# Kernel optimization log

Measured on AMD Instinct MI355X. Metric: run time of the kernel, lower is better.

The kernel has to match this reference:

```python
import jax, jax.numpy as jnp
import numpy as np
from jax import lax

B, N = 8, 32768
N_G, N_C, K = 256, 64, 16
n_G, k_ = 16, 4          # sqrt(N_G), sqrt(K)
M, m_ = N_G * K, n_G * k_
EPS = 1e-6


def _w(key, i, o):
    return jax.random.normal(key, (i, o), jnp.float32) * (1.0 / np.sqrt(i))


def setup_inputs() -> dict:
    key = jax.random.key(0)
    ks = jax.random.split(key, 16)
    return {
        "pts": jax.random.normal(ks[0], (B, N, 3), jnp.float32),
        # G2SD: PointNet encoder (3->128->256, maxpool) + folding decoder (2+256 -> 256 -> 3)
        "ge_w1": _w(ks[1], 3, 128),   "ge_b1": jnp.zeros((128,), jnp.float32),
        "ge_w2": _w(ks[2], 128, 256), "ge_b2": jnp.zeros((256,), jnp.float32),
        "gd_w1": _w(ks[3], 258, 256), "gd_b1": jnp.zeros((256,), jnp.float32),
        "gd_w2": _w(ks[4], 256, 3),   "gd_b2": jnp.zeros((3,), jnp.float32),
        # S2PF: per-point encoder (3->128, maxpool) + per-point flattener (3+128 -> 128 -> 2)
        "se_w1": _w(ks[5], 3, 128),   "se_b1": jnp.zeros((128,), jnp.float32),
        "sd_w1": _w(ks[6], 131, 128), "sd_b1": jnp.zeros((128,), jnp.float32),
        "sd_w2": _w(ks[7], 128, 2),   "sd_b2": jnp.zeros((2,), jnp.float32),
    }


def _sqdist(a, b):
    # a [B,P,3], b [B,Q,3] -> [B,P,Q]
    return (jnp.sum(a * a, -1)[:, :, None] + jnp.sum(b * b, -1)[:, None, :]
            - 2.0 * jnp.einsum('bpd,bqd->bpq', a, b))


def fps(pts, n):
    Bb, Nn, _ = pts.shape
    def step(carry, _):
        dist, cur = carry
        sel = pts[jnp.arange(Bb), cur]                       # [B,3]
        d = jnp.sum((pts - sel[:, None, :]) ** 2, -1)        # [B,N]
        dist = jnp.minimum(dist, d)
        nxt = jnp.argmax(dist, -1).astype(jnp.int32)
        return (dist, nxt), cur
    init = (jnp.full((Bb, Nn), 1e10, pts.dtype), jnp.zeros((Bb,), jnp.int32))
    _, idx = lax.scan(step, init, None, length=n)            # [n,B]
    return idx.T                                             # [B,n]


def index_points(pts, idx):
    # pts [B,N,3], idx [B,...] -> [B,...,3]
    return jax.vmap(lambda p, i: p[i])(pts, idx)


def _grid(nn):
    lin = (jnp.arange(nn, dtype=jnp.float32) + 0.5) / nn
    gy, gx = jnp.meshgrid(lin, lin, indexing='ij')
    return jnp.stack([gx, gy], -1).reshape(nn * nn, 2)       # row-major [nn*nn,2]


def g2sd(pts_g, ge_w1, ge_b1, ge_w2, ge_b2, gd_w1, gd_b1, gd_w2, gd_b2):
    h = jax.nn.relu(pts_g @ ge_w1 + ge_b1)
    h = jax.nn.relu(h @ ge_w2 + ge_b2)
    code = jnp.max(h, axis=1)                                # [B,256]
    grid = jnp.broadcast_to(_grid(n_G)[None], (pts_g.shape[0], N_G, 2))
    feat = jnp.concatenate([grid, jnp.broadcast_to(code[:, None, :], (pts_g.shape[0], N_G, 256))], -1)
    h2 = jax.nn.relu(feat @ gd_w1 + gd_b1)
    return h2 @ gd_w2 + gd_b2                                # [B,N_G,3]


def s2pf(x, se_w1, se_b1, sd_w1, sd_b1, sd_w2, sd_b2):
    # x [BG, N_C, 3] -> 2D embedding [BG, N_C, 2]
    h = jax.nn.relu(x @ se_w1 + se_b1)
    code = jnp.max(h, axis=1)                                # [BG,128]
    f = jnp.concatenate([x, jnp.broadcast_to(code[:, None, :], (x.shape[0], x.shape[1], 128))], -1)
    h2 = jax.nn.relu(f @ sd_w1 + sd_b1)
    return h2 @ sd_w2 + sd_b2


def normalize_anchor_patches(pts_c):
    c = jnp.mean(pts_c, axis=2, keepdims=True)
    x = pts_c - c
    s = jnp.max(jnp.linalg.norm(x, axis=-1), axis=-1)[..., None, None]
    return x / (s + 1e-8)


def rescale_pe(pe, lo, hi):
    mn = jnp.min(pe, axis=1, keepdims=True)
    mx = jnp.max(pe, axis=1, keepdims=True)
    return (pe - mn) / (mx - mn + 1e-8) * (hi - lo) + lo


def reference(pts, ge_w1, ge_b1, ge_w2, ge_b2, gd_w1, gd_b1, gd_w2, gd_b2,
              se_w1, se_b1, sd_w1, sd_b1, sd_w2, sd_b2):
    Bb = pts.shape[0]
    # 1) FPS -> anchor points, G2SD -> grid-ordered reconstruction
    pts_g = index_points(pts, fps(pts, N_G))                 # [B,N_G,3]
    rec_g = g2sd(pts_g, ge_w1, ge_b1, ge_w2, ge_b2, gd_w1, gd_b1, gd_w2, gd_b2)
    # 2) KNN patches around each grid anchor
    d = _sqdist(rec_g, pts)                                  # [B,N_G,N]
    _, knn_idx = lax.top_k(-d, N_C)                          # [B,N_G,N_C]
    pts_c = index_points(pts, knn_idx)                       # [B,N_G,N_C,3]
    # 3) Local flattening to 2D embeddings in (0,1)^2
    pts_c_n = normalize_anchor_patches(pts_c)
    pe = s2pf(pts_c_n.reshape(Bb * N_G, N_C, 3), se_w1, se_b1, sd_w1, sd_b1, sd_w2, sd_b2)
    ebd_c = rescale_pe(pe, EPS, 1.0 - EPS).reshape(Bb, N_G, N_C, 2)
    # 4) Per-patch grid resample: nearest embedded point per k x k grid cell
    gK = _grid(k_)                                           # [K,2]
    d2 = jnp.sum((gK[None, None, :, None, :] - ebd_c[:, :, None, :, :]) ** 2, -1)  # [B,N_G,K,N_C]
    near = jnp.argmin(d2, axis=-1)                           # [B,N_G,K]
    pgi_local = jnp.take_along_axis(pts_c, jnp.broadcast_to(near[..., None], (Bb, N_G, K, 3)), axis=2)
    # 5) Assemble n_G x n_G patches of k x k cells into [B,3,m,m], flatten to [B,M,3]
    img = pgi_local.reshape(Bb, n_G, n_G, k_, k_, 3).transpose(0, 5, 1, 3, 2, 4).reshape(Bb, 3, m_, m_)
    return img.reshape(Bb, 3, M).transpose(0, 2, 1)          # [B,M,3]
```

## Files before the change

kernel.cpp:

```cpp
#include <hip/hip_runtime.h>

#define NPTS 32768
#define NB 8
#define NG 256

__global__ __launch_bounds__(1024, 4) void k_fps(const float* __restrict__ pts,
                                                 float* __restrict__ ptsg) {
  const int b = blockIdx.x;
  const int t = threadIdx.x;
  const float* __restrict__ P = pts + (size_t)b * NPTS * 3;
  __shared__ float Dl[NPTS];
  float cx[32], cy[32], cz[32];
#pragma unroll
  for (int i = 0; i < 32; ++i) {
    int p = i * 1024 + t;
    cx[i] = P[p * 3 + 0];
    cy[i] = P[p * 3 + 1];
    cz[i] = P[p * 3 + 2];
  }
  __shared__ float rv[16];
  __shared__ int ri[16];
  __shared__ int scur;
  int cur = 0;
  for (int it = 0; it < NG; ++it) {
    float sx = P[cur * 3 + 0], sy = P[cur * 3 + 1], sz = P[cur * 3 + 2];
    if (t == 0) {
      float* G = ptsg + ((size_t)b * NG + it) * 3;
      G[0] = sx; G[1] = sy; G[2] = sz;
    }
    float bv = -1.0f;
    int bi = 0x7fffffff;
#pragma unroll
    for (int i = 0; i < 32; ++i) {
      int p = i * 1024 + t;
      float dx = __fsub_rn(cx[i], sx), dy = __fsub_rn(cy[i], sy), dz = __fsub_rn(cz[i], sz);
      float d = __fadd_rn(__fadd_rn(__fmul_rn(dx, dx), __fmul_rn(dy, dy)),
                          __fmul_rn(dz, dz));
      float nd = d;
      if (it > 0) nd = fminf(Dl[p], d);
      Dl[p] = nd;
      if (nd > bv || (nd == bv && p < bi)) { bv = nd; bi = p; }
    }
    for (int off = 32; off > 0; off >>= 1) {
      float ov = __shfl_down(bv, off);
      int oi = __shfl_down(bi, off);
      if (ov > bv || (ov == bv && oi < bi)) { bv = ov; bi = oi; }
    }
    int wid = t >> 6, lane = t & 63;
    if (lane == 0) { rv[wid] = bv; ri[wid] = bi; }
    __syncthreads();
    if (t < 64) {
      float v = (t < 16) ? rv[t] : -2.0f;
      int ix = (t < 16) ? ri[t] : 0x7fffffff;
      for (int off = 8; off > 0; off >>= 1) {
        float ov = __shfl_down(v, off);
        int oi = __shfl_down(ix, off);
        if (ov > v || (ov == v && oi < ix)) { v = ov; ix = oi; }
      }
      if (t == 0) scur = ix;
    }
    __syncthreads();
    cur = scur;
  }
}

__global__ __launch_bounds__(256) void k_enc1(const float* __restrict__ ptsg,
                                              const float* __restrict__ w1,
                                              const float* __restrict__ b1,
                                              float* __restrict__ h1) {
  int gid = blockIdx.x * 256 + threadIdx.x;
  int f = gid & 127;
  int p = gid >> 7;
  const float* x = ptsg + (size_t)p * 3;
  float acc = __fmul_rn(x[0], w1[0 * 128 + f]);
  acc = fmaf(x[1], w1[1 * 128 + f], acc);
  acc = fmaf(x[2], w1[2 * 128 + f], acc);
  h1[gid] = fmaxf(__fadd_rn(acc, b1[f]), 0.0f);
}

__global__ __launch_bounds__(256) void k_code(const float* __restrict__ h1,
                                              const float* __restrict__ w2,
                                              const float* __restrict__ b2,
                                              float* __restrict__ codeG) {
  int b = blockIdx.x;
  int j = threadIdx.x;
  float m = -__builtin_inff();
  for (int p = 0; p < 256; ++p) {
    const float* hrow = h1 + ((size_t)b * 256 + p) * 128;
    float acc = __fmul_rn(hrow[0], w2[0 * 256 + j]);
    for (int f = 1; f < 128; ++f)
      acc = fmaf(hrow[f], w2[f * 256 + j], acc);
    float v = fmaxf(__fadd_rn(acc, b2[j]), 0.0f);
    m = fmaxf(m, v);
  }
  codeG[b * 256 + j] = m;
}

__global__ __launch_bounds__(256) void k_dec(const float* __restrict__ codeG,
                                             const float* __restrict__ w1,
                                             const float* __restrict__ b1,
                                             const float* __restrict__ w2,
                                             const float* __restrict__ b2,
                                             float* __restrict__ recg) {
  int blk = blockIdx.x;
  int b = blk >> 8, g = blk & 255;
  int f = threadIdx.x;
  float gx = (float)((((double)(g & 15)) + 0.5) / 16.0);
  float gy = (float)((((double)(g >> 4)) + 0.5) / 16.0);
  const float* code = codeG + b * 256;
  float acc = __fmul_rn(gx, w1[0 * 256 + f]);
  acc = fmaf(gy, w1[1 * 256 + f], acc);
  for (int c = 0; c < 256; ++c)
    acc = fmaf(code[c], w1[(2 + c) * 256 + f], acc);
  float a = fmaxf(__fadd_rn(acc, b1[f]), 0.0f);
  __shared__ float hs[256];
  hs[f] = a;
  __syncthreads();
  if (f < 3) {
    float acc2 = __fmul_rn(hs[0], w2[0 * 3 + f]);
    for (int k = 1; k < 256; ++k)
      acc2 = fmaf(hs[k], w2[k * 3 + f], acc2);
    recg[blk * 3 + f] = __fadd_rn(acc2, b2[f]);
  }
}

__global__ __launch_bounds__(1024) void k_knn(const float* __restrict__ pts,
                                              const float* __restrict__ recg,
                                              float* __restrict__ ptsc) {
  int bg = blockIdx.x;
  int b = bg >> 8;
  int t = threadIdx.x;
  const float* __restrict__ P = pts + (size_t)b * NPTS * 3;
  float qx = recg[bg * 3 + 0];
  float qy = recg[bg * 3 + 1];
  float qz = recg[bg * 3 + 2];
  float ra = __fadd_rn(__fadd_rn(__fmul_rn(qx, qx), __fmul_rn(qy, qy)),
                       __fmul_rn(qz, qz));
  unsigned kk[32];
#pragma unroll
  for (int i = 0; i < 32; ++i) {
    int p = i * 1024 + t;
    float px = P[p * 3], py = P[p * 3 + 1], pz = P[p * 3 + 2];
    float rb = __fadd_rn(__fadd_rn(__fmul_rn(px, px), __fmul_rn(py, py)),
                         __fmul_rn(pz, pz));
    float ab = fmaf(qz, pz, fmaf(qy, py, __fmul_rn(qx, px)));
    float d = __fsub_rn(__fadd_rn(ra, rb), __fmul_rn(2.0f, ab));
    unsigned u = __float_as_uint(d);
    u = (u & 0x80000000u) ? ~u : (u | 0x80000000u);
    kk[i] = u;
  }
  __shared__ unsigned hist[2048];
  __shared__ unsigned s_bin, s_cum;
  __shared__ unsigned s_cntlt, s_cnteq;
  __shared__ unsigned candU[64];
  __shared__ int candI[64];
  __shared__ int eqI_[192];

  unsigned prefix = 0, pmask = 0;
  int rank = 64;
#pragma unroll
  for (int pass = 0; pass < 3; ++pass) {
    const int shift = (pass == 0) ? 21 : (pass == 1) ? 10 : 0;
    const unsigned bm = (pass == 2) ? 1023u : 2047u;
    hist[t] = 0u;
    hist[t + 1024] = 0u;
    __syncthreads();
#pragma unroll
    for (int i = 0; i < 32; ++i) {
      unsigned u = kk[i];
      if ((u & pmask) == prefix) atomicAdd(&hist[(u >> shift) & bm], 1u);
    }
    __syncthreads();
    if (t < 64) {
      int base = t * 32;
      unsigned ls = 0;
      for (int k2 = 0; k2 < 32; ++k2) ls += hist[base + k2];
      unsigned incl = ls;
      for (int off = 1; off < 64; off <<= 1) {
        unsigned v = __shfl_up(incl, off);
        if (t >= off) incl += v;
      }
      unsigned excl = incl - ls;
      if ((int)excl < rank && rank <= (int)incl) {
        unsigned c = excl;
        int binf = base;
        for (int k2 = 0; k2 < 32; ++k2) {
          unsigned h = hist[base + k2];
          if ((int)(c + h) >= rank) { binf = base + k2; break; }
          c += h;
        }
        s_bin = (unsigned)binf;
        s_cum = c;
      }
    }
    __syncthreads();
    rank -= (int)s_cum;
    prefix |= (s_bin & bm) << shift;
    pmask |= bm << shift;
  }
  unsigned usel = prefix;
  if (t == 0) { s_cntlt = 0; s_cnteq = 0; }
  __syncthreads();
#pragma unroll
  for (int i = 0; i < 32; ++i) {
    unsigned u = kk[i];
    int p = i * 1024 + t;
    if (u < usel) {
      unsigned pos = atomicAdd(&s_cntlt, 1u);
      candU[pos] = u; candI[pos] = p;
    } else if (u == usel) {
      unsigned pos = atomicAdd(&s_cnteq, 1u);
      if (pos < 192u) eqI_[pos] = p;
    }
  }
  __syncthreads();
  if (t == 0) {
    int cl = (int)s_cntlt;
    int ne = (int)s_cnteq; if (ne > 192) ne = 192;
    int need = 64 - cl;
    for (int n = 0; n < need; ++n) {
      int bmin = 0x7fffffff, bk2 = -1;
      for (int k2 = 0; k2 < ne; ++k2)
        if (eqI_[k2] < bmin) { bmin = eqI_[k2]; bk2 = k2; }
      candU[cl + n] = usel; candI[cl + n] = bmin;
      if (bk2 >= 0) eqI_[bk2] = 0x7fffffff;
    }
  }
  __syncthreads();
  if (t < 64) {
    unsigned mu = candU[t];
    int mi = candI[t];
    int r = 0;
    for (int k2 = 0; k2 < 64; ++k2) {
      unsigned ou = candU[k2]; int oi = candI[k2];
      if (ou < mu || (ou == mu && oi < mi)) ++r;
    }
    float* o = ptsc + ((size_t)bg * 64 + r) * 3;
    o[0] = P[mi * 3]; o[1] = P[mi * 3 + 1]; o[2] = P[mi * 3 + 2];
  }
}

__device__ inline float wmaxf(float v) {
  for (int off = 1; off < 64; off <<= 1) v = fmaxf(v, __shfl_xor(v, off));
  return v;
}
__device__ inline float wminf(float v) {
  for (int off = 1; off < 64; off <<= 1) v = fminf(v, __shfl_xor(v, off));
  return v;
}

__global__ __launch_bounds__(64) void k_patch(const float* __restrict__ ptsc,
                                              const float* __restrict__ se_w1,
                                              const float* __restrict__ se_b1,
                                              const float* __restrict__ sd_w1,
                                              const float* __restrict__ sd_b1,
                                              const float* __restrict__ sd_w2,
                                              const float* __restrict__ sd_b2,
                                              float* __restrict__ out) {
  int bg = blockIdx.x;
  int b = bg >> 8, g = bg & 255;
  int j = threadIdx.x;
  __shared__ float pc[64][3];
  __shared__ float xn[64][3];
  __shared__ float code[128];
  __shared__ float cmean[3];
  __shared__ float earr[64][2];
  const float* src = ptsc + ((size_t)bg * 64 + j) * 3;
  float p0 = src[0], p1 = src[1], p2 = src[2];
  pc[j][0] = p0; pc[j][1] = p1; pc[j][2] = p2;
  __syncthreads();
  if (j < 3) {
    float sum = pc[0][j];
    for (int k = 1; k < 64; ++k) sum = __fadd_rn(sum, pc[k][j]);
    cmean[j] = __fdiv_rn(sum, 64.0f);
  }
  __syncthreads();
  float x0 = __fsub_rn(p0, cmean[0]);
  float x1 = __fsub_rn(p1, cmean[1]);
  float x2 = __fsub_rn(p2, cmean[2]);
  float nr = sqrtf(__fadd_rn(__fadd_rn(__fmul_rn(x0, x0), __fmul_rn(x1, x1)),
                             __fmul_rn(x2, x2)));
  float s = wmaxf(nr);
  float den = __fadd_rn(s, 1e-8f);
  x0 = __fdiv_rn(x0, den);
  x1 = __fdiv_rn(x1, den);
  x2 = __fdiv_rn(x2, den);
  xn[j][0] = x0; xn[j][1] = x1; xn[j][2] = x2;
  __syncthreads();
  for (int ff = 0; ff < 2; ++ff) {
    int f = j + ff * 64;
    float w0 = se_w1[0 * 128 + f];
    float w1v = se_w1[1 * 128 + f];
    float w2v = se_w1[2 * 128 + f];
    float bb = se_b1[f];
    float m = -__builtin_inff();
    for (int p = 0; p < 64; ++p) {
      float acc = __fmul_rn(xn[p][0], w0);
      acc = fmaf(xn[p][1], w1v, acc);
      acc = fmaf(xn[p][2], w2v, acc);
      float v = fmaxf(__fadd_rn(acc, bb), 0.0f);
      m = fmaxf(m, v);
    }
    code[f] = m;
  }
  __syncthreads();
  float pe0 = 0.0f, pe1 = 0.0f;
  for (int f = 0; f < 128; ++f) {
    float acc = __fmul_rn(x0, sd_w1[0 * 128 + f]);
    acc = fmaf(x1, sd_w1[1 * 128 + f], acc);
    acc = fmaf(x2, sd_w1[2 * 128 + f], acc);
    for (int c = 0; c < 128; ++c)
      acc = fmaf(code[c], sd_w1[(3 + c) * 128 + f], acc);
    float h = fmaxf(__fadd_rn(acc, sd_b1[f]), 0.0f);
    if (f == 0) {
      pe0 = __fmul_rn(h, sd_w2[0 * 2 + 0]);
      pe1 = __fmul_rn(h, sd_w2[0 * 2 + 1]);
    } else {
      pe0 = fmaf(h, sd_w2[f * 2 + 0], pe0);
      pe1 = fmaf(h, sd_w2[f * 2 + 1], pe1);
    }
  }
  pe0 = __fadd_rn(pe0, sd_b2[0]);
  pe1 = __fadd_rn(pe1, sd_b2[1]);
  float mn0 = wminf(pe0), mx0 = wmaxf(pe0);
  float mn1 = wminf(pe1), mx1 = wmaxf(pe1);
  const float SPAN = (float)0.999998;
  float e0 = __fadd_rn(__fmul_rn(__fdiv_rn(__fsub_rn(pe0, mn0),
                                           __fadd_rn(__fsub_rn(mx0, mn0), 1e-8f)),
                                 SPAN), 1e-6f);
  float e1 = __fadd_rn(__fmul_rn(__fdiv_rn(__fsub_rn(pe1, mn1),
                                           __fadd_rn(__fsub_rn(mx1, mn1), 1e-8f)),
                                 SPAN), 1e-6f);
  earr[j][0] = e0;
  earr[j][1] = e1;
  __syncthreads();
  if (j < 16) {
    float gxf = (float)((((double)(j & 3)) + 0.5) * 0.25);
    float gyf = (float)((((double)(j >> 2)) + 0.5) * 0.25);
    float best = __builtin_inff();
    int bi = 0;
    for (int sslot = 0; sslot < 64; ++sslot) {
      float dx = __fsub_rn(gxf, earr[sslot][0]);
      float dy = __fsub_rn(gyf, earr[sslot][1]);
      float d2 = __fadd_rn(__fmul_rn(dx, dx), __fmul_rn(dy, dy));
      if (d2 < best) { best = d2; bi = sslot; }
    }
    int rr = (g >> 4) * 4 + (j >> 2);
    int cc = (g & 15) * 4 + (j & 3);
    float* o = out + (((size_t)b * 4096) + (size_t)(rr * 64 + cc)) * 3;
    o[0] = pc[bi][0]; o[1] = pc[bi][1]; o[2] = pc[bi][2];
  }
}

extern "C" void kernel_launch(void* const* d_in, const int* in_sizes, int n_in,
                              void* d_out, int out_size, void* d_ws, size_t ws_size,
                              hipStream_t stream) {
  const float* pts   = (const float*)d_in[0];
  const float* ge_w1 = (const float*)d_in[1];
  const float* ge_b1 = (const float*)d_in[2];
  const float* ge_w2 = (const float*)d_in[3];
  const float* ge_b2 = (const float*)d_in[4];
  const float* gd_w1 = (const float*)d_in[5];
  const float* gd_b1 = (const float*)d_in[6];
  const float* gd_w2 = (const float*)d_in[7];
  const float* gd_b2 = (const float*)d_in[8];
  const float* se_w1 = (const float*)d_in[9];
  const float* se_b1 = (const float*)d_in[10];
  const float* sd_w1 = (const float*)d_in[11];
  const float* sd_b1 = (const float*)d_in[12];
  const float* sd_w2 = (const float*)d_in[13];
  const float* sd_b2 = (const float*)d_in[14];
  float* out = (float*)d_out;

  float* ws    = (float*)d_ws;
  float* h1    = ws;
  float* codeG = h1 + 262144;
  float* recg  = codeG + 2048;
  float* ptsg  = recg + 6144;
  float* ptsc  = ptsg + 6144;

  k_fps<<<NB, 1024, 0, stream>>>(pts, ptsg);
  k_enc1<<<(NB * NG * 128) / 256, 256, 0, stream>>>(ptsg, ge_w1, ge_b1, h1);
  k_code<<<NB, 256, 0, stream>>>(h1, ge_w2, ge_b2, codeG);
  k_dec<<<NB * NG, 256, 0, stream>>>(codeG, gd_w1, gd_b1, gd_w2, gd_b2, recg);
  k_knn<<<NB * NG, 1024, 0, stream>>>(pts, recg, ptsc);
  k_patch<<<NB * NG, 64, 0, stream>>>(ptsc, se_w1, se_b1, sd_w1, sd_b1, sd_w2, sd_b2, out);
}
```

Measured before the change: 3.224 ms.

## Rework FPS, k_code, kNN radix select and patch MLP loops

FPS keeps 12 points per thread in registers and re-reads the rest as contiguous float4 global loads each iteration, using double-buffered reduction slots so one barrier per iteration is removed. k_code splits the 256 points across four thread groups and combines their maxima through shared memory, giving more parallelism per batch. The kNN radix select moves to four 8-bit passes with per-wave histograms to reduce atomic contention. The patch kernel unrolls its max-pool and register-blocks the decoder matmul eight features at a time. The trade-off is extra global traffic in FPS and one more select pass in kNN.

```diff
diff --git a/kernel.cpp b/kernel.cpp
--- a/kernel.cpp
+++ b/kernel.cpp
@@ -3,24 +3,28 @@
 #define NPTS 32768
 #define NB 8
 #define NG 256
+#define REGPTS 12
+#define RELPTS 20
+#define RELBASE (REGPTS * 1024)
 
 __global__ __launch_bounds__(1024, 4) void k_fps(const float* __restrict__ pts,
                                                  float* __restrict__ ptsg) {
   const int b = blockIdx.x;
   const int t = threadIdx.x;
   const float* __restrict__ P = pts + (size_t)b * NPTS * 3;
+  const float4* __restrict__ P4 =
+      reinterpret_cast<const float4*>(P + (size_t)RELBASE * 3);
   __shared__ float Dl[NPTS];
-  float cx[32], cy[32], cz[32];
-#pragma unroll
-  for (int i = 0; i < 32; ++i) {
+  __shared__ float rv[2][16];
+  __shared__ int ri[2][16];
+  float cx[REGPTS], cy[REGPTS], cz[REGPTS];
+#pragma unroll
+  for (int i = 0; i < REGPTS; ++i) {
     int p = i * 1024 + t;
     cx[i] = P[p * 3 + 0];
     cy[i] = P[p * 3 + 1];
     cz[i] = P[p * 3 + 2];
   }
-  __shared__ float rv[16];
-  __shared__ int ri[16];
-  __shared__ int scur;
   int cur = 0;
   for (int it = 0; it < NG; ++it) {
     float sx = P[cur * 3 + 0], sy = P[cur * 3 + 1], sz = P[cur * 3 + 2];
@@ -31,7 +35,7 @@
     float bv = -1.0f;
     int bi = 0x7fffffff;
 #pragma unroll
-    for (int i = 0; i < 32; ++i) {
+    for (int i = 0; i < REGPTS; ++i) {
       int p = i * 1024 + t;
       float dx = __fsub_rn(cx[i], sx), dy = __fsub_rn(cy[i], sy), dz = __fsub_rn(cz[i], sz);
       float d = __fadd_rn(__fadd_rn(__fmul_rn(dx, dx), __fmul_rn(dy, dy)),
@@ -41,26 +45,46 @@
       Dl[p] = nd;
       if (nd > bv || (nd == bv && p < bi)) { bv = nd; bi = p; }
     }
+#pragma unroll
+    for (int g = 0; g < 5; ++g) {
+      float4 q0 = P4[t * 15 + g * 3 + 0];
+      float4 q1 = P4[t * 15 + g * 3 + 1];
+      float4 q2 = P4[t * 15 + g * 3 + 2];
+      float xs[12] = {q0.x, q0.y, q0.z, q0.w, q1.x, q1.y, q1.z, q1.w,
+                      q2.x, q2.y, q2.z, q2.w};
+#pragma unroll
+      for (int j = 0; j < 4; ++j) {
+        int p = RELBASE + t * RELPTS + g * 4 + j;
+        float dx = __fsub_rn(xs[j * 3 + 0], sx);
+        float dy = __fsub_rn(xs[j * 3 + 1], sy);
+        float dz = __fsub_rn(xs[j * 3 + 2], sz);
+        float d = __fadd_rn(__fadd_rn(__fmul_rn(dx, dx), __fmul_rn(dy, dy)),
+                            __fmul_rn(dz, dz));
+        float nd = d;
+        if (it > 0) nd = fminf(Dl[p], d);
+        Dl[p] = nd;
+        if (nd > bv || (nd == bv && p < bi)) { bv = nd; bi = p; }
+      }
+    }
     for (int off = 32; off > 0; off >>= 1) {
       float ov = __shfl_down(bv, off);
       int oi = __shfl_down(bi, off);
       if (ov > bv || (ov == bv && oi < bi)) { bv = ov; bi = oi; }
     }
+    int par = it & 1;
     int wid = t >> 6, lane = t & 63;
-    if (lane == 0) { rv[wid] = bv; ri[wid] = bi; }
+    if (lane == 0) { rv[par][wid] = bv; ri[par][wid] = bi; }
     __syncthreads();
-    if (t < 64) {
-      float v = (t < 16) ? rv[t] : -2.0f;
-      int ix = (t < 16) ? ri[t] : 0x7fffffff;
+    {
+      float v = (lane < 16) ? rv[par][lane] : -2.0f;
+      int ix = (lane < 16) ? ri[par][lane] : 0x7fffffff;
       for (int off = 8; off > 0; off >>= 1) {
         float ov = __shfl_down(v, off);
         int oi = __shfl_down(ix, off);
         if (ov > v || (ov == v && oi < ix)) { v = ov; ix = oi; }
       }
-      if (t == 0) scur = ix;
-    }
-    __syncthreads();
-    cur = scur;
+      cur = __shfl(ix, 0);
+    }
   }
 }
 
@@ -78,14 +102,17 @@
   h1[gid] = fmaxf(__fadd_rn(acc, b1[f]), 0.0f);
 }
 
-__global__ __launch_bounds__(256) void k_code(const float* __restrict__ h1,
-                                              const float* __restrict__ w2,
-                                              const float* __restrict__ b2,
-                                              float* __restrict__ codeG) {
+__global__ __launch_bounds__(1024) void k_code(const float* __restrict__ h1,
+                                               const float* __restrict__ w2,
+                                               const float* __restrict__ b2,
+                                               float* __restrict__ codeG) {
   int b = blockIdx.x;
-  int j = threadIdx.x;
+  int t = threadIdx.x;
+  int j = t & 255;
+  int q = t >> 8;
+  __shared__ float part[4][256];
   float m = -__builtin_inff();
-  for (int p = 0; p < 256; ++p) {
+  for (int p = q * 64; p < q * 64 + 64; ++p) {
     const float* hrow = h1 + ((size_t)b * 256 + p) * 128;
     float acc = __fmul_rn(hrow[0], w2[0 * 256 + j]);
     for (int f = 1; f < 128; ++f)
@@ -93,7 +120,11 @@
     float v = fmaxf(__fadd_rn(acc, b2[j]), 0.0f);
     m = fmaxf(m, v);
   }
-  codeG[b * 256 + j] = m;
+  part[q][j] = m;
+  __syncthreads();
+  if (q == 0)
+    codeG[b * 256 + j] =
+        fmaxf(fmaxf(part[0][j], part[1][j]), fmaxf(part[2][j], part[3][j]));
 }
 
 __global__ __launch_bounds__(256) void k_dec(const float* __restrict__ codeG,
@@ -149,32 +180,39 @@
     u = (u & 0x80000000u) ? ~u : (u | 0x80000000u);
     kk[i] = u;
   }
-  __shared__ unsigned hist[2048];
+  __shared__ unsigned whist[16][256];
+  __shared__ unsigned chist[256];
   __shared__ unsigned s_bin, s_cum;
   __shared__ unsigned s_cntlt, s_cnteq;
   __shared__ unsigned candU[64];
   __shared__ int candI[64];
   __shared__ int eqI_[192];
+  int wid = t >> 6;
 
   unsigned prefix = 0, pmask = 0;
   int rank = 64;
 #pragma unroll
-  for (int pass = 0; pass < 3; ++pass) {
-    const int shift = (pass == 0) ? 21 : (pass == 1) ? 10 : 0;
-    const unsigned bm = (pass == 2) ? 1023u : 2047u;
-    hist[t] = 0u;
-    hist[t + 1024] = 0u;
+  for (int pass = 0; pass < 4; ++pass) {
+    const int shift = 24 - 8 * pass;
+    unsigned* wh = &whist[0][0];
+    for (int k2 = t; k2 < 16 * 256; k2 += 1024) wh[k2] = 0u;
     __syncthreads();
 #pragma unroll
     for (int i = 0; i < 32; ++i) {
       unsigned u = kk[i];
-      if ((u & pmask) == prefix) atomicAdd(&hist[(u >> shift) & bm], 1u);
+      if ((u & pmask) == prefix)
+        atomicAdd(&whist[wid][(u >> shift) & 255u], 1u);
+    }
+    __syncthreads();
+    if (t < 256) {
+      unsigned s = 0;
+      for (int w = 0; w < 16; ++w) s += whist[w][t];
+      chist[t] = s;
     }
     __syncthreads();
     if (t < 64) {
-      int base = t * 32;
-      unsigned ls = 0;
-      for (int k2 = 0; k2 < 32; ++k2) ls += hist[base + k2];
+      int base = t * 4;
+      unsigned ls = chist[base] + chist[base + 1] + chist[base + 2] + chist[base + 3];
       unsigned incl = ls;
       for (int off = 1; off < 64; off <<= 1) {
         unsigned v = __shfl_up(incl, off);
@@ -184,8 +222,8 @@
       if ((int)excl < rank && rank <= (int)incl) {
         unsigned c = excl;
         int binf = base;
-        for (int k2 = 0; k2 < 32; ++k2) {
-          unsigned h = hist[base + k2];
+        for (int k2 = 0; k2 < 4; ++k2) {
+          unsigned h = chist[base + k2];
           if ((int)(c + h) >= rank) { binf = base + k2; break; }
           c += h;
         }
@@ -195,8 +233,8 @@
     }
     __syncthreads();
     rank -= (int)s_cum;
-    prefix |= (s_bin & bm) << shift;
-    pmask |= bm << shift;
+    prefix |= (s_bin & 255u) << shift;
+    pmask |= 255u << shift;
   }
   unsigned usel = prefix;
   if (t == 0) { s_cntlt = 0; s_cnteq = 0; }
@@ -293,31 +331,48 @@
     float w1v = se_w1[1 * 128 + f];
     float w2v = se_w1[2 * 128 + f];
     float bb = se_b1[f];
-    float m = -__builtin_inff();
-    for (int p = 0; p < 64; ++p) {
-      float acc = __fmul_rn(xn[p][0], w0);
-      acc = fmaf(xn[p][1], w1v, acc);
-      acc = fmaf(xn[p][2], w2v, acc);
-      float v = fmaxf(__fadd_rn(acc, bb), 0.0f);
-      m = fmaxf(m, v);
-    }
-    code[f] = m;
+    float m0 = -__builtin_inff(), m1 = -__builtin_inff();
+    float m2 = -__builtin_inff(), m3 = -__builtin_inff();
+    for (int p = 0; p < 64; p += 4) {
+      float a0 = fmaf(xn[p + 0][2], w2v, fmaf(xn[p + 0][1], w1v, __fmul_rn(xn[p + 0][0], w0)));
+      float a1 = fmaf(xn[p + 1][2], w2v, fmaf(xn[p + 1][1], w1v, __fmul_rn(xn[p + 1][0], w0)));
+      float a2 = fmaf(xn[p + 2][2], w2v, fmaf(xn[p + 2][1], w1v, __fmul_rn(xn[p + 2][0], w0)));
+      float a3 = fmaf(xn[p + 3][2], w2v, fmaf(xn[p + 3][1], w1v, __fmul_rn(xn[p + 3][0], w0)));
+      m0 = fmaxf(m0, fmaxf(__fadd_rn(a0, bb), 0.0f));
+      m1 = fmaxf(m1, fmaxf(__fadd_rn(a1, bb), 0.0f));
+      m2 = fmaxf(m2, fmaxf(__fadd_rn(a2, bb), 0.0f));
+      m3 = fmaxf(m3, fmaxf(__fadd_rn(a3, bb), 0.0f));
+    }
+    code[f] = fmaxf(fmaxf(m0, m1), fmaxf(m2, m3));
   }
   __syncthreads();
   float pe0 = 0.0f, pe1 = 0.0f;
-  for (int f = 0; f < 128; ++f) {
-    float acc = __fmul_rn(x0, sd_w1[0 * 128 + f]);
-    acc = fmaf(x1, sd_w1[1 * 128 + f], acc);
-    acc = fmaf(x2, sd_w1[2 * 128 + f], acc);
-    for (int c = 0; c < 128; ++c)
-      acc = fmaf(code[c], sd_w1[(3 + c) * 128 + f], acc);
-    float h = fmaxf(__fadd_rn(acc, sd_b1[f]), 0.0f);
-    if (f == 0) {
-      pe0 = __fmul_rn(h, sd_w2[0 * 2 + 0]);
-      pe1 = __fmul_rn(h, sd_w2[0 * 2 + 1]);
-    } else {
-      pe0 = fmaf(h, sd_w2[f * 2 + 0], pe0);
-      pe1 = fmaf(h, sd_w2[f * 2 + 1], pe1);
+  for (int f0 = 0; f0 < 128; f0 += 8) {
+    float a[8];
+#pragma unroll
+    for (int u = 0; u < 8; ++u) {
+      int f = f0 + u;
+      float acc = __fmul_rn(x0, sd_w1[0 * 128 + f]);
+      acc = fmaf(x1, sd_w1[1 * 128 + f], acc);
+      a[u] = fmaf(x2, sd_w1[2 * 128 + f], acc);
+    }
+    for (int c = 0; c < 128; ++c) {
+      float cv = code[c];
+      const float* wrow = sd_w1 + (3 + c) * 128 + f0;
+#pragma unroll
+      for (int u = 0; u < 8; ++u) a[u] = fmaf(cv, wrow[u], a[u]);
+    }
+#pragma unroll
+    for (int u = 0; u < 8; ++u) {
+      int f = f0 + u;
+      float h = fmaxf(__fadd_rn(a[u], sd_b1[f]), 0.0f);
+      if (f == 0) {
+        pe0 = __fmul_rn(h, sd_w2[0 * 2 + 0]);
+        pe1 = __fmul_rn(h, sd_w2[0 * 2 + 1]);
+      } else {
+        pe0 = fmaf(h, sd_w2[f * 2 + 0], pe0);
+        pe1 = fmaf(h, sd_w2[f * 2 + 1], pe1);
+      }
     }
   }
   pe0 = __fadd_rn(pe0, sd_b2[0]);
@@ -381,7 +436,7 @@
 
   k_fps<<<NB, 1024, 0, stream>>>(pts, ptsg);
   k_enc1<<<(NB * NG * 128) / 256, 256, 0, stream>>>(ptsg, ge_w1, ge_b1, h1);
-  k_code<<<NB, 256, 0, stream>>>(h1, ge_w2, ge_b2, codeG);
+  k_code<<<NB, 1024, 0, stream>>>(h1, ge_w2, ge_b2, codeG);
   k_dec<<<NB * NG, 256, 0, stream>>>(codeG, gd_w1, gd_b1, gd_w2, gd_b2, recg);
   k_knn<<<NB * NG, 1024, 0, stream>>>(pts, recg, ptsc);
   k_patch<<<NB * NG, 64, 0, stream>>>(ptsc, se_w1, se_b1, sd_w1, sd_b1, sd_w2, sd_b2, out);
```

New measurement: 2.869 ms. -11.0%, faster.
